# Kernel tuning notes

Hardware: AMD Instinct MI355X
Metric: run time of the kernel (lower is better)

Reference implementation:

```python
import jax, jax.numpy as jnp
import numpy as np

D = 1024
H = 4
HD = D // H
WIN = 128
NPMEM = 4
EPS = 1e-5


def _layernorm(x, g, b):
    mu = jnp.mean(x, axis=-1, keepdims=True)
    var = jnp.var(x, axis=-1, keepdims=True)
    return (x - mu) * jax.lax.rsqrt(var + EPS) * g + b


def _rotate_half(t):
    h = t.shape[-1] // 2
    return jnp.concatenate([-t[..., h:], t[..., :h]], axis=-1)


def setup_inputs() -> dict:
    key = jax.random.key(0)
    ks = jax.random.split(key, 20)
    B, L = 2, 4096
    s = 0.02
    inp = {
        'x': jax.random.normal(ks[0], (B, L, D), jnp.float32),
        'cos': jax.random.uniform(ks[1], (L + 8, HD), jnp.float32),
        'sin': jax.random.uniform(ks[2], (L + 8, HD), jnp.float32),
        'global_out': jax.random.normal(ks[3], (B, L, D), jnp.float32),
        'local_out': jax.random.normal(ks[4], (B, L, D), jnp.float32),
        'wq': jax.random.normal(ks[5], (D, D), jnp.float32) * s,
        'wk': jax.random.normal(ks[6], (D, D), jnp.float32) * s,
        'wv': jax.random.normal(ks[7], (D, D), jnp.float32) * s,
        'wo_attn': jax.random.normal(ks[8], (D, D), jnp.float32) * s,
        'pmem': jax.random.normal(ks[9], (1, NPMEM, D), jnp.float32),
        'gate_w': jax.random.normal(ks[10], (3 * D, 3 * D), jnp.float32) * s,
        'gate_b': jnp.zeros((3 * D,), jnp.float32),
        'outproj_w': jax.random.normal(ks[11], (3 * D, D), jnp.float32) * s,
        'outproj_b': jnp.zeros((D,), jnp.float32),
        'ln_mem_g': jnp.ones((D,), jnp.float32),
        'ln_mem_b': jnp.zeros((D,), jnp.float32),
        'ln_mlp_g': jnp.ones((D,), jnp.float32),
        'ln_mlp_b': jnp.zeros((D,), jnp.float32),
        'fc1_w': jax.random.normal(ks[12], (D, 4 * D), jnp.float32) * s,
        'fc1_b': jnp.zeros((4 * D,), jnp.float32),
        'fc2_w': jax.random.normal(ks[13], (4 * D, D), jnp.float32) * s,
        'fc2_b': jnp.zeros((D,), jnp.float32),
    }
    return inp


def reference(x, cos, sin, global_out, local_out, wq, wk, wv, wo_attn, pmem,
              gate_w, gate_b, outproj_w, outproj_b, ln_mem_g, ln_mem_b,
              ln_mlp_g, ln_mlp_b, fc1_w, fc1_b, fc2_w, fc2_b):
    B, L, _ = x.shape
    residual = x

    # prepend persistent memory tokens
    xp = jnp.concatenate([jnp.broadcast_to(pmem, (B, NPMEM, D)), x], axis=1)
    Lt = L + NPMEM

    q = (xp @ wq).reshape(B, Lt, H, HD)
    k = (xp @ wk).reshape(B, Lt, H, HD)
    v = (xp @ wv).reshape(B, Lt, H, HD)

    # rotary embedding over the full pmem+seq length
    cc = cos[:Lt][None, :, None, :]
    ss = sin[:Lt][None, :, None, :]
    q = q * cc + _rotate_half(q) * ss
    k = k * cc + _rotate_half(k) * ss

    i = jnp.arange(Lt)[:, None]
    j = jnp.arange(Lt)[None, :]
    mask = (j <= i) & (j >= i - WIN)  # [Lt, Lt]

    scale = 1.0 / jnp.sqrt(jnp.asarray(HD, x.dtype))
    scores = jnp.einsum('blhd,bmhd->bhlm', q, k) * scale
    scores = jnp.where(mask[None, None], scores, jnp.finfo(scores.dtype).min)
    attn = jax.nn.softmax(scores, axis=-1)
    out = jnp.einsum('bhlm,bmhd->blhd', attn, v).reshape(B, Lt, D)
    core_out = (out @ wo_attn)[:, -L:, :]

    combined = jnp.concatenate([global_out, local_out, core_out], axis=-1)
    g = jax.nn.sigmoid(combined @ gate_w + gate_b)
    memory_output = (combined * g) @ outproj_w + outproj_b

    x1 = residual + _layernorm(memory_output, ln_mem_g, ln_mem_b)
    xn = _layernorm(x1, ln_mlp_g, ln_mlp_b)
    mlp_out = jax.nn.silu(xn @ fc1_w + fc1_b) @ fc2_w + fc2_b
    return x1 + mlp_out
```

## Files before the change

### kernel.cpp

```cpp
#include <hip/hip_runtime.h>
#include <stdint.h>

#define D_    1024
#define H_    4
#define HD_   256
#define WIN_  128
#define NPM_  4
#define B_    2
#define L_    4096
#define LT_   4100
#define LTP_  4112
#define QKL_  3072

typedef __attribute__((ext_vector_type(8))) short short8;
typedef __attribute__((ext_vector_type(4))) float f32x4;

__device__ __forceinline__ short f2bf(float f) {
  union { float f; uint32_t u; } v; v.f = f;
  uint32_t r = v.u + 0x7FFFu + ((v.u >> 16) & 1u);
  return (short)(r >> 16);
}
__device__ __forceinline__ float bf2f(short h) {
  union { uint32_t u; float f; } v; v.u = ((uint32_t)(uint16_t)h) << 16;
  return v.f;
}

typedef __attribute__((address_space(1))) void GAS;
typedef __attribute__((address_space(3))) void LAS;
__device__ __forceinline__ void gl16(const void* g, void* l) {
  __builtin_amdgcn_global_load_lds((GAS*)g, (LAS*)l, 16, 0, 0);
}
__device__ __forceinline__ void waitvm0() { asm volatile("s_waitcnt vmcnt(0)" ::: "memory"); }

#define EP_BF16 0
#define EP_F32B 1
#define EP_GATE 2
#define EP_SILU 3
#define EP_RES  4
#define EP_CORE 5

template<int EP, int TM>
__global__ __launch_bounds__(256, 2)
void gemm_bt(const short* __restrict__ A, int lda,
             const short* __restrict__ Bt,
             void* __restrict__ Cp, int ldc,
             const float* __restrict__ bias,
             const void* __restrict__ aux, int ldaux,
             int M, int N, int K)
{
  constexpr int WM = TM / 2;
  constexpr int MT = WM / 16;
  constexpr int BUFSZ = (TM + 128) * 32;
  __shared__ __attribute__((aligned(16))) short lds[2 * BUFSZ];
  const int tid  = threadIdx.x;
  const int lane = tid & 63, wave = tid >> 6;
  const int lhi  = lane >> 4, llo = lane & 15;
  const int m0 = blockIdx.x * TM, n0 = blockIdx.y * 128;
  const int mw = (wave >> 1) * WM, nw = (wave & 1) * 64;

  const int srow = tid >> 2;
  const int sg   = (tid & 3) ^ ((tid >> 3) & 3);
  const short* pA0 = A + (size_t)min(m0 + srow, M - 1) * lda + sg * 8;
  const short* pA1 = (TM == 128) ? A + (size_t)min(m0 + srow + 64, M - 1) * lda + sg * 8 : pA0;
  const short* pB0 = Bt + (size_t)(n0 + srow) * K + sg * 8;
  const short* pB1 = Bt + (size_t)(n0 + srow + 64) * K + sg * 8;

  const int segoff = (lhi ^ ((llo >> 1) & 3)) * 8;

  auto stage = [&](int b, int i) {
    const int k = i << 5;
    short* base = &lds[b * BUFSZ];
    gl16(pA0 + k, &base[tid * 8]);
    if constexpr (TM == 128) gl16(pA1 + k, &base[2048 + tid * 8]);
    gl16(pB0 + k, &base[TM * 32 + tid * 8]);
    gl16(pB1 + k, &base[TM * 32 + 2048 + tid * 8]);
  };

  f32x4 acc[MT][4];
#pragma unroll
  for (int i = 0; i < MT; i++)
#pragma unroll
    for (int j = 0; j < 4; j++) acc[i][j] = f32x4{0.f, 0.f, 0.f, 0.f};

  const int NI = K >> 5;
  stage(0, 0);
  waitvm0();
  __syncthreads();

  for (int i = 0; i < NI; i++) {
    if (i + 1 < NI) stage((i + 1) & 1, i + 1);
    const short* bufp = &lds[(i & 1) * BUFSZ];
    short8 af[MT], bfr[4];
#pragma unroll
    for (int mt = 0; mt < MT; mt++)
      af[mt] = *(const short8*)&bufp[(mw + mt * 16 + llo) * 32 + segoff];
#pragma unroll
    for (int nt = 0; nt < 4; nt++)
      bfr[nt] = *(const short8*)&bufp[TM * 32 + (nw + nt * 16 + llo) * 32 + segoff];
#pragma unroll
    for (int mt = 0; mt < MT; mt++)
#pragma unroll
      for (int nt = 0; nt < 4; nt++)
        acc[mt][nt] = __builtin_amdgcn_mfma_f32_16x16x32_bf16(af[mt], bfr[nt], acc[mt][nt], 0, 0, 0);
    waitvm0();
    __syncthreads();
  }

  const int gcb = n0 + nw;
#pragma unroll
  for (int mt = 0; mt < MT; mt++) {
    const int gr0 = m0 + mw + mt * 16 + lhi * 4;
#pragma unroll
    for (int nt = 0; nt < 4; nt++) {
      const int gc = gcb + nt * 16 + llo;
      float bv = 0.f;
      if constexpr (EP != EP_BF16 && EP != EP_CORE) bv = bias[gc];
#pragma unroll
      for (int r = 0; r < 4; r++) {
        const int gr = gr0 + r;
        if (gr >= M) continue;
        const float v = acc[mt][nt][r];
        if constexpr (EP == EP_CORE) {
          const int b   = gr >= LT_ ? 1 : 0;
          const int tok = gr - b * LT_;
          if (tok >= NPM_) {
            const int cr = b * L_ + (tok - NPM_);
            ((short*)Cp)[(size_t)cr * ldc + gc] = f2bf(v);
          }
          continue;
        }
        const size_t idx = (size_t)gr * ldc + gc;
        if constexpr (EP == EP_BF16) {
          ((short*)Cp)[idx] = f2bf(v);
        } else if constexpr (EP == EP_F32B) {
          ((float*)Cp)[idx] = v + bv;
        } else if constexpr (EP == EP_GATE) {
          float g  = 1.f / (1.f + __expf(-(v + bv)));
          float cv = bf2f(((const short*)aux)[(size_t)gr * ldaux + gc]);
          ((short*)Cp)[idx] = f2bf(cv * g);
        } else if constexpr (EP == EP_SILU) {
          float xx = v + bv;
          ((short*)Cp)[idx] = f2bf(xx / (1.f + __expf(-xx)));
        } else {
          ((float*)Cp)[idx] = v + bv + ((const float*)aux)[(size_t)gr * ldaux + gc];
        }
      }
    }
  }
}

struct TAll {
  const float* src[8];
  short* dst[8];
  int C[8];
  int R[8];
  int nbx[8];
  int start[8];
};

__global__ __launch_bounds__(256)
void transpose_all(TAll t)
{
  __shared__ short tile[32][33];
  const int bid = blockIdx.x;
  int w = 0;
#pragma unroll
  for (int i = 1; i < 8; i++) w = (bid >= t.start[i]) ? i : w;
  const int rel = bid - t.start[w];
  const int nbx = t.nbx[w];
  const int bx = rel % nbx, by = rel / nbx;
  const float* src = t.src[w];
  short* dst = t.dst[w];
  const int ld_in = t.C[w], ld_out = t.R[w];
  const int r0 = by * 32, c0 = bx * 32;
  const int tx = threadIdx.x & 31, ty = threadIdx.x >> 5;
#pragma unroll
  for (int i = 0; i < 4; i++)
    tile[ty + i * 8][tx] = f2bf(src[(size_t)(r0 + ty + i * 8) * ld_in + c0 + tx]);
  __syncthreads();
#pragma unroll
  for (int i = 0; i < 4; i++)
    dst[(size_t)(c0 + ty + i * 8) * ld_out + r0 + tx] = tile[tx][ty + i * 8];
}

template<typename Tin>
__global__ __launch_bounds__(256)
void cast_transpose(const Tin* __restrict__ in, short* __restrict__ outp,
                    int R, int C, int ld_in, int ld_out,
                    int zdiv, size_t inA, size_t inB, size_t outA, size_t outB)
{
  __shared__ short tile[32][33];
  const int z = blockIdx.z;
  const Tin* src = in + (size_t)(z / zdiv) * inA + (size_t)(z % zdiv) * inB;
  short* dst = outp + (size_t)(z / zdiv) * outA + (size_t)(z % zdiv) * outB;
  const int r0 = blockIdx.y * 32, c0 = blockIdx.x * 32;
  const int tx = threadIdx.x & 31, ty = threadIdx.x >> 5;
#pragma unroll
  for (int i = 0; i < 4; i++) {
    int r = r0 + ty + i * 8, c = c0 + tx;
    short v = 0;
    if (r < R && c < C) {
      if constexpr (sizeof(Tin) == 4) v = f2bf((float)src[(size_t)r * ld_in + c]);
      else                            v = (short)src[(size_t)r * ld_in + c];
    }
    tile[ty + i * 8][tx] = v;
  }
  __syncthreads();
#pragma unroll
  for (int i = 0; i < 4; i++) {
    int c = c0 + ty + i * 8, r = r0 + tx;
    if (c < C && r < R) dst[(size_t)c * ld_out + r] = tile[tx][ty + i * 8];
  }
}

__global__ __launch_bounds__(256)
void build_xp_k(const float* __restrict__ x, const float* __restrict__ pmem,
                short* __restrict__ xp)
{
  int gid = blockIdx.x * 256 + threadIdx.x;
  int row = gid >> 8;
  int c4  = (gid & 255) * 4;
  int b   = row >= LT_ ? 1 : 0;
  int tok = row - b * LT_;
  const float* src = (tok < NPM_) ? (pmem + (size_t)tok * D_ + c4)
                                  : (x + ((size_t)b * L_ + tok - NPM_) * D_ + c4);
  float4 v = *(const float4*)src;
  short o[4] = {f2bf(v.x), f2bf(v.y), f2bf(v.z), f2bf(v.w)};
  *(short4*)&xp[(size_t)row * D_ + c4] = *(short4*)o;
}

__global__ __launch_bounds__(256)
void combined01_k(const float* __restrict__ go, const float* __restrict__ lo,
                  short* __restrict__ comb)
{
  int gid = blockIdx.x * 256 + threadIdx.x;
  int row = gid >> 9;
  int c4  = (gid & 511) * 4;
  const float* src = (c4 < D_) ? (go + (size_t)row * D_ + c4)
                               : (lo + (size_t)row * D_ + (c4 - D_));
  float4 v = *(const float4*)src;
  short o[4] = {f2bf(v.x), f2bf(v.y), f2bf(v.z), f2bf(v.w)};
  *(short4*)&comb[(size_t)row * 3072 + c4] = *(short4*)o;
}

__global__ __launch_bounds__(256)
void rope_kernel(short* __restrict__ qkv,
                 const float* __restrict__ cosp, const float* __restrict__ sinp)
{
  int gid = blockIdx.x * 256 + threadIdx.x;
  int d   = (gid & 31) * 4;
  int h   = (gid >> 5) & 3;
  int row = gid >> 7;
  int t   = row >= LT_ ? row - LT_ : row;
  size_t base = (size_t)row * QKL_ + h * HD_ + d;
  float4 cl = *(const float4*)&cosp[(size_t)t * HD_ + d];
  float4 ch = *(const float4*)&cosp[(size_t)t * HD_ + d + 128];
  float4 sl = *(const float4*)&sinp[(size_t)t * HD_ + d];
  float4 sh = *(const float4*)&sinp[(size_t)t * HD_ + d + 128];
  short4 ql4 = *(const short4*)&qkv[base],        qh4 = *(const short4*)&qkv[base + 128];
  short4 kl4 = *(const short4*)&qkv[base + 1024], kh4 = *(const short4*)&qkv[base + 1152];
  const float SC = 1.f / 16.f;
  short oql[4], oqh[4], okl[4], okh[4];
#pragma unroll
  for (int j = 0; j < 4; j++) {
    float c0 = ((float*)&cl)[j], c1 = ((float*)&ch)[j];
    float s0 = ((float*)&sl)[j], s1 = ((float*)&sh)[j];
    float ql = bf2f(((short*)&ql4)[j]), qh = bf2f(((short*)&qh4)[j]);
    float kl = bf2f(((short*)&kl4)[j]), kh = bf2f(((short*)&kh4)[j]);
    oql[j] = f2bf((ql * c0 - qh * s0) * SC);
    oqh[j] = f2bf((qh * c1 + ql * s1) * SC);
    okl[j] = f2bf(kl * c0 - kh * s0);
    okh[j] = f2bf(kh * c1 + kl * s1);
  }
  *(short4*)&qkv[base]        = *(short4*)oql;
  *(short4*)&qkv[base + 128]  = *(short4*)oqh;
  *(short4*)&qkv[base + 1024] = *(short4*)okl;
  *(short4*)&qkv[base + 1152] = *(short4*)okh;
}

__global__ __launch_bounds__(256, 1)
void attn_kernel(const short* __restrict__ qkv, const short* __restrict__ vT,
                 short* __restrict__ outp)
{
  __shared__ short lKV[256 * 72];
  __shared__ short lP[64 * 200];
  const int tid  = threadIdx.x;
  const int lane = tid & 63, wave = tid >> 6;
  const int lhi  = lane >> 4, llo = lane & 15;
  const int i0 = blockIdx.x * 64;
  const int h = blockIdx.y, b = blockIdx.z;
  const int kw0 = i0 - 128;
  const size_t vbase = (size_t)(b * H_ + h) * HD_ * LTP_;

  short8 qf[8];
  {
    int ic = min(i0 + wave * 16 + llo, LT_ - 1);
    const short* qrow = qkv + (size_t)(b * LT_ + ic) * QKL_ + h * HD_;
#pragma unroll
    for (int ks = 0; ks < 8; ks++)
      qf[ks] = *(const short8*)(qrow + ks * 32 + lhi * 8);
  }

  f32x4 S[12];
#pragma unroll
  for (int st = 0; st < 12; st++) S[st] = f32x4{0.f, 0.f, 0.f, 0.f};

  for (int kc = 0; kc < 3; kc++) {
    if (kc) __syncthreads();
    {
      int row = tid >> 2;
      int jc = min(max(kw0 + kc * 64 + row, 0), LT_ - 1);
      const short* krow = qkv + (size_t)(b * LT_ + jc) * QKL_ + 1024 + h * HD_;
#pragma unroll
      for (int it = 0; it < 8; it++) {
        int seg = (tid & 3) + it * 4;
        *(short8*)&lKV[row * 264 + seg * 8] = *(const short8*)(krow + seg * 8);
      }
    }
    __syncthreads();
#pragma unroll
    for (int ks = 0; ks < 8; ks++) {
#pragma unroll
      for (int nt = 0; nt < 4; nt++) {
        short8 bf = *(const short8*)&lKV[(nt * 16 + llo) * 264 + ks * 32 + lhi * 8];
        S[kc * 4 + nt] = __builtin_amdgcn_mfma_f32_16x16x32_bf16(qf[ks], bf, S[kc * 4 + nt], 0, 0, 0);
      }
    }
  }

  const int irow = i0 + wave * 16 + lhi * 4;
  float mx[4], sm[4];
#pragma unroll
  for (int r = 0; r < 4; r++) mx[r] = -3.0e38f;
#pragma unroll
  for (int st = 0; st < 12; st++) {
    int j = kw0 + st * 16 + llo;
#pragma unroll
    for (int r = 0; r < 4; r++) {
      int i = irow + r;
      bool ok = (j >= 0) & (j <= i) & (j >= i - WIN_);
      float s = ok ? S[st][r] : -1.0e30f;
      S[st][r] = s;
      mx[r] = fmaxf(mx[r], s);
    }
  }
#pragma unroll
  for (int r = 0; r < 4; r++)
#pragma unroll
    for (int o = 1; o < 16; o <<= 1) mx[r] = fmaxf(mx[r], __shfl_xor(mx[r], o));
#pragma unroll
  for (int r = 0; r < 4; r++) sm[r] = 0.f;
#pragma unroll
  for (int st = 0; st < 12; st++)
#pragma unroll
    for (int r = 0; r < 4; r++) {
      float e = __expf(S[st][r] - mx[r]);
      S[st][r] = e;
      sm[r] += e;
    }
#pragma unroll
  for (int r = 0; r < 4; r++) {
#pragma unroll
    for (int o = 1; o < 16; o <<= 1) sm[r] += __shfl_xor(sm[r], o);
    sm[r] = 1.f / sm[r];
  }

#pragma unroll
  for (int st = 0; st < 12; st++)
#pragma unroll
    for (int r = 0; r < 4; r++)
      lP[(wave * 16 + lhi * 4 + r) * 200 + st * 16 + llo] = f2bf(S[st][r] * sm[r]);

  f32x4 O[16];
#pragma unroll
  for (int nt = 0; nt < 16; nt++) O[nt] = f32x4{0.f, 0.f, 0.f, 0.f};

  for (int kc = 0; kc < 3; kc++) {
    __syncthreads();
#pragma unroll
    for (int it = 0; it < 8; it++) {
      int id = it * 256 + tid;
      int d = id >> 3, seg = id & 7;
      int kbase = min(max(kw0 + kc * 64 + seg * 8, 0), LTP_ - 8);
      *(short8*)&lKV[d * 72 + seg * 8] = *(const short8*)&vT[vbase + (size_t)d * LTP_ + kbase];
    }
    __syncthreads();
#pragma unroll
    for (int ks = 0; ks < 2; ks++) {
      short8 pf = *(const short8*)&lP[(wave * 16 + llo) * 200 + kc * 64 + ks * 32 + lhi * 8];
#pragma unroll
      for (int nt = 0; nt < 16; nt++) {
        short8 vf = *(const short8*)&lKV[(nt * 16 + llo) * 72 + ks * 32 + lhi * 8];
        O[nt] = __builtin_amdgcn_mfma_f32_16x16x32_bf16(pf, vf, O[nt], 0, 0, 0);
      }
    }
  }

  short* orow = outp + (size_t)(b * LT_) * D_ + h * HD_;
#pragma unroll
  for (int nt = 0; nt < 16; nt++)
#pragma unroll
    for (int r = 0; r < 4; r++) {
      int i = irow + r;
      if (i < LT_) orow[(size_t)i * D_ + nt * 16 + llo] = f2bf(O[nt][r]);
    }
}

__global__ __launch_bounds__(256, 4)
void ln2_kernel(const float* __restrict__ mo, const float* __restrict__ xres,
                const float* __restrict__ g1, const float* __restrict__ b1,
                const float* __restrict__ g2, const float* __restrict__ b2,
                float* __restrict__ x1, short* __restrict__ xn)
{
  const int row = blockIdx.x;
  const int tid = threadIdx.x;
  const int lane = tid & 63, wave = tid >> 6;
  __shared__ float red[8], red2[8];
  float4 v = ((const float4*)(mo + (size_t)row * D_))[tid];
  float s = v.x + v.y + v.z + v.w;
  float s2 = v.x * v.x + v.y * v.y + v.z * v.z + v.w * v.w;
#pragma unroll
  for (int o = 1; o < 64; o <<= 1) { s += __shfl_xor(s, o); s2 += __shfl_xor(s2, o); }
  if (lane == 0) { red[wave] = s; red[wave + 4] = s2; }
  __syncthreads();
  float S = red[0] + red[1] + red[2] + red[3];
  float S2 = red[4] + red[5] + red[6] + red[7];
  float mu = S * (1.f / D_);
  float rs = rsqrtf(S2 * (1.f / D_) - mu * mu + 1e-5f);
  float4 gg = ((const float4*)g1)[tid];
  float4 bb = ((const float4*)b1)[tid];
  float4 xv = ((const float4*)(xres + (size_t)row * D_))[tid];
  float4 o1;
  o1.x = xv.x + (v.x - mu) * rs * gg.x + bb.x;
  o1.y = xv.y + (v.y - mu) * rs * gg.y + bb.y;
  o1.z = xv.z + (v.z - mu) * rs * gg.z + bb.z;
  o1.w = xv.w + (v.w - mu) * rs * gg.w + bb.w;
  ((float4*)(x1 + (size_t)row * D_))[tid] = o1;
  s = o1.x + o1.y + o1.z + o1.w;
  s2 = o1.x * o1.x + o1.y * o1.y + o1.z * o1.z + o1.w * o1.w;
#pragma unroll
  for (int o = 1; o < 64; o <<= 1) { s += __shfl_xor(s, o); s2 += __shfl_xor(s2, o); }
  if (lane == 0) { red2[wave] = s; red2[wave + 4] = s2; }
  __syncthreads();
  S = red2[0] + red2[1] + red2[2] + red2[3];
  S2 = red2[4] + red2[5] + red2[6] + red2[7];
  float mu2 = S * (1.f / D_);
  float rs2 = rsqrtf(S2 * (1.f / D_) - mu2 * mu2 + 1e-5f);
  float4 g2v = ((const float4*)g2)[tid];
  float4 b2v = ((const float4*)b2)[tid];
  short o2[4];
  o2[0] = f2bf((o1.x - mu2) * rs2 * g2v.x + b2v.x);
  o2[1] = f2bf((o1.y - mu2) * rs2 * g2v.y + b2v.y);
  o2[2] = f2bf((o1.z - mu2) * rs2 * g2v.z + b2v.z);
  o2[3] = f2bf((o1.w - mu2) * rs2 * g2v.w + b2v.w);
  *(short4*)&xn[(size_t)row * D_ + tid * 4] = *(short4*)o2;
}

extern "C" void kernel_launch(void* const* d_in, const int* in_sizes, int n_in,
                              void* d_out, int out_size, void* d_ws, size_t ws_size,
                              hipStream_t stream)
{
  const float* x      = (const float*)d_in[0];
  const float* cosp   = (const float*)d_in[1];
  const float* sinp   = (const float*)d_in[2];
  const float* go     = (const float*)d_in[3];
  const float* lo     = (const float*)d_in[4];
  const float* wq     = (const float*)d_in[5];
  const float* wk     = (const float*)d_in[6];
  const float* wv     = (const float*)d_in[7];
  const float* wo     = (const float*)d_in[8];
  const float* pmem   = (const float*)d_in[9];
  const float* gate_w = (const float*)d_in[10];
  const float* gate_b = (const float*)d_in[11];
  const float* outp_w = (const float*)d_in[12];
  const float* outp_b = (const float*)d_in[13];
  const float* ln1g   = (const float*)d_in[14];
  const float* ln1b   = (const float*)d_in[15];
  const float* ln2g   = (const float*)d_in[16];
  const float* ln2b   = (const float*)d_in[17];
  const float* fc1w   = (const float*)d_in[18];
  const float* fc1b   = (const float*)d_in[19];
  const float* fc2w   = (const float*)d_in[20];
  const float* fc2b   = (const float*)d_in[21];
  float* out = (float*)d_out;
  char* p = (char*)d_ws;

  short* wqkvT = (short*)(p + 0);
  short* woT   = (short*)(p + 6291456);
  short* gateT = (short*)(p + 8388608);
  short* outpT = (short*)(p + 27262976);
  short* fc1T  = (short*)(p + 33554432);
  short* fc2T  = (short*)(p + 41943040);
  short* comb  = (short*)(p + 50331648);
  char*  pool  = p + 100663296;
  short* xp    = (short*)(pool);
  short* qkv   = (short*)(pool + 16793600);
  short* vT    = (short*)(pool + 67174400);
  short* a_o   = (short*)(pool + 84017152);
  short* gated = (short*)(pool);
  short* h1    = (short*)(pool);
  float* mo    = (float*)(pool + 67174400);
  float* x1    = (float*)(comb);
  short* xn    = (short*)((char*)comb + 33554432);

  TAll t;
  const float* srcs[8] = {wq, wk, wv, wo, gate_w, outp_w, fc1w, fc2w};
  short* dsts[8] = {wqkvT, wqkvT + 1048576, wqkvT + 2097152, woT, gateT, outpT, fc1T, fc2T};
  const int Rs[8] = {1024, 1024, 1024, 1024, 3072, 3072, 1024, 4096};
  const int Cs[8] = {1024, 1024, 1024, 1024, 3072, 1024, 4096, 1024};
  int cum = 0;
  for (int i = 0; i < 8; i++) {
    t.src[i] = srcs[i]; t.dst[i] = dsts[i];
    t.R[i] = Rs[i]; t.C[i] = Cs[i]; t.nbx[i] = Cs[i] / 32;
    t.start[i] = cum;
    cum += (Cs[i] / 32) * (Rs[i] / 32);
  }
  transpose_all<<<cum, 256, 0, stream>>>(t);

  build_xp_k<<<8200, 256, 0, stream>>>(x, pmem, xp);
  combined01_k<<<16384, 256, 0, stream>>>(go, lo, comb);

  const int Mq = B_ * LT_;
  gemm_bt<EP_BF16, 128><<<dim3(65, 24), 256, 0, stream>>>(xp, 1024, wqkvT, qkv, QKL_, nullptr, nullptr, 0, Mq, 3072, 1024);

  rope_kernel<<<4100, 256, 0, stream>>>(qkv, cosp, sinp);
  cast_transpose<short><<<dim3(8, 129, 8), 256, 0, stream>>>(
      qkv + 2048, vT, LT_, 256, QKL_, LTP_, 4,
      (size_t)LT_ * QKL_, 256, (size_t)4 * 256 * LTP_, (size_t)256 * LTP_);

  attn_kernel<<<dim3(65, H_, B_), 256, 0, stream>>>(qkv, vT, a_o);

  gemm_bt<EP_CORE, 64><<<dim3(129, 8), 256, 0, stream>>>(
      a_o, 1024, woT, comb + 2048, 3072, nullptr, nullptr, 0, Mq, 1024, 1024);

  gemm_bt<EP_GATE, 128><<<dim3(64, 24), 256, 0, stream>>>(comb, 3072, gateT, gated, 3072, gate_b, comb, 3072, 8192, 3072, 3072);

  gemm_bt<EP_F32B, 64><<<dim3(128, 8), 256, 0, stream>>>(gated, 3072, outpT, mo, 1024, outp_b, nullptr, 0, 8192, 1024, 3072);

  ln2_kernel<<<8192, 256, 0, stream>>>(mo, x, ln1g, ln1b, ln2g, ln2b, x1, xn);

  gemm_bt<EP_SILU, 128><<<dim3(64, 32), 256, 0, stream>>>(xn, 1024, fc1T, h1, 4096, fc1b, nullptr, 0, 8192, 4096, 1024);
  gemm_bt<EP_RES, 64><<<dim3(128, 8), 256, 0, stream>>>(h1, 4096, fc2T, out, 1024, fc2b, x1, 1024, 8192, 1024, 4096);
}
```

Measured before the change: 972.2 us.

## Compute V transposed directly via swapped GEMM and fuse prep kernels

The V projection is split out of the fused QKV GEMM and computed as Wv^T · xp^T, with a new epilogue that writes straight into the head-major transposed V buffer. This removes the separate cast_transpose pass and the V columns of the qkv buffer. The two input-conversion kernels are merged into one launch, and the launch-bounds occupancy hints for the GEMM and attention kernels are raised. The transposed-store epilogue writes with strided scatter, and the higher occupancy hints may cause register spills.

```diff
diff --git a/kernel.cpp b/kernel.cpp
--- a/kernel.cpp
+++ b/kernel.cpp
@@ -10,7 +10,7 @@
 #define L_    4096
 #define LT_   4100
 #define LTP_  4112
-#define QKL_  3072
+#define QKL_  2048
 
 typedef __attribute__((ext_vector_type(8))) short short8;
 typedef __attribute__((ext_vector_type(4))) float f32x4;
@@ -38,9 +38,10 @@
 #define EP_SILU 3
 #define EP_RES  4
 #define EP_CORE 5
+#define EP_VT   6
 
 template<int EP, int TM>
-__global__ __launch_bounds__(256, 2)
+__global__ __launch_bounds__(256, 4)
 void gemm_bt(const short* __restrict__ A, int lda,
              const short* __restrict__ Bt,
              void* __restrict__ Cp, int ldc,
@@ -114,12 +115,21 @@
     for (int nt = 0; nt < 4; nt++) {
       const int gc = gcb + nt * 16 + llo;
       float bv = 0.f;
-      if constexpr (EP != EP_BF16 && EP != EP_CORE) bv = bias[gc];
+      if constexpr (EP != EP_BF16 && EP != EP_CORE && EP != EP_VT) bv = bias[gc];
 #pragma unroll
       for (int r = 0; r < 4; r++) {
         const int gr = gr0 + r;
         if (gr >= M) continue;
         const float v = acc[mt][nt][r];
+        if constexpr (EP == EP_VT) {
+          if (gc < N) {
+            const int b   = gc >= LT_ ? 1 : 0;
+            const int tok = gc - b * LT_;
+            const int hh  = gr >> 8, dd = gr & 255;
+            ((short*)Cp)[(size_t)((b * H_ + hh) * HD_ + dd) * ldc + tok] = f2bf(v);
+          }
+          continue;
+        }
         if constexpr (EP == EP_CORE) {
           const int b   = gr >= LT_ ? 1 : 0;
           const int tok = gr - b * LT_;
@@ -183,64 +193,33 @@
     dst[(size_t)(c0 + ty + i * 8) * ld_out + r0 + tx] = tile[tx][ty + i * 8];
 }
 
-template<typename Tin>
 __global__ __launch_bounds__(256)
-void cast_transpose(const Tin* __restrict__ in, short* __restrict__ outp,
-                    int R, int C, int ld_in, int ld_out,
-                    int zdiv, size_t inA, size_t inB, size_t outA, size_t outB)
-{
-  __shared__ short tile[32][33];
-  const int z = blockIdx.z;
-  const Tin* src = in + (size_t)(z / zdiv) * inA + (size_t)(z % zdiv) * inB;
-  short* dst = outp + (size_t)(z / zdiv) * outA + (size_t)(z % zdiv) * outB;
-  const int r0 = blockIdx.y * 32, c0 = blockIdx.x * 32;
-  const int tx = threadIdx.x & 31, ty = threadIdx.x >> 5;
-#pragma unroll
-  for (int i = 0; i < 4; i++) {
-    int r = r0 + ty + i * 8, c = c0 + tx;
-    short v = 0;
-    if (r < R && c < C) {
-      if constexpr (sizeof(Tin) == 4) v = f2bf((float)src[(size_t)r * ld_in + c]);
-      else                            v = (short)src[(size_t)r * ld_in + c];
-    }
-    tile[ty + i * 8][tx] = v;
-  }
-  __syncthreads();
-#pragma unroll
-  for (int i = 0; i < 4; i++) {
-    int c = c0 + ty + i * 8, r = r0 + tx;
-    if (c < C && r < R) dst[(size_t)c * ld_out + r] = tile[tx][ty + i * 8];
-  }
-}
-
-__global__ __launch_bounds__(256)
-void build_xp_k(const float* __restrict__ x, const float* __restrict__ pmem,
-                short* __restrict__ xp)
-{
-  int gid = blockIdx.x * 256 + threadIdx.x;
-  int row = gid >> 8;
-  int c4  = (gid & 255) * 4;
-  int b   = row >= LT_ ? 1 : 0;
-  int tok = row - b * LT_;
-  const float* src = (tok < NPM_) ? (pmem + (size_t)tok * D_ + c4)
-                                  : (x + ((size_t)b * L_ + tok - NPM_) * D_ + c4);
-  float4 v = *(const float4*)src;
-  short o[4] = {f2bf(v.x), f2bf(v.y), f2bf(v.z), f2bf(v.w)};
-  *(short4*)&xp[(size_t)row * D_ + c4] = *(short4*)o;
-}
-
-__global__ __launch_bounds__(256)
-void combined01_k(const float* __restrict__ go, const float* __restrict__ lo,
-                  short* __restrict__ comb)
-{
-  int gid = blockIdx.x * 256 + threadIdx.x;
-  int row = gid >> 9;
-  int c4  = (gid & 511) * 4;
-  const float* src = (c4 < D_) ? (go + (size_t)row * D_ + c4)
-                               : (lo + (size_t)row * D_ + (c4 - D_));
-  float4 v = *(const float4*)src;
-  short o[4] = {f2bf(v.x), f2bf(v.y), f2bf(v.z), f2bf(v.w)};
-  *(short4*)&comb[(size_t)row * 3072 + c4] = *(short4*)o;
+void prep_k(const float* __restrict__ x, const float* __restrict__ pmem,
+            const float* __restrict__ go, const float* __restrict__ lo,
+            short* __restrict__ xp, short* __restrict__ comb)
+{
+  const int bid = blockIdx.x;
+  if (bid < 8200) {
+    int gid = bid * 256 + threadIdx.x;
+    int row = gid >> 8;
+    int c4  = (gid & 255) * 4;
+    int b   = row >= LT_ ? 1 : 0;
+    int tok = row - b * LT_;
+    const float* src = (tok < NPM_) ? (pmem + (size_t)tok * D_ + c4)
+                                    : (x + ((size_t)b * L_ + tok - NPM_) * D_ + c4);
+    float4 v = *(const float4*)src;
+    short o[4] = {f2bf(v.x), f2bf(v.y), f2bf(v.z), f2bf(v.w)};
+    *(short4*)&xp[(size_t)row * D_ + c4] = *(short4*)o;
+  } else {
+    int gid = (bid - 8200) * 256 + threadIdx.x;
+    int row = gid >> 9;
+    int c4  = (gid & 511) * 4;
+    const float* src = (c4 < D_) ? (go + (size_t)row * D_ + c4)
+                                 : (lo + (size_t)row * D_ + (c4 - D_));
+    float4 v = *(const float4*)src;
+    short o[4] = {f2bf(v.x), f2bf(v.y), f2bf(v.z), f2bf(v.w)};
+    *(short4*)&comb[(size_t)row * 3072 + c4] = *(short4*)o;
+  }
 }
 
 __global__ __launch_bounds__(256)
@@ -278,7 +257,7 @@
   *(short4*)&qkv[base + 1152] = *(short4*)okh;
 }
 
-__global__ __launch_bounds__(256, 1)
+__global__ __launch_bounds__(256, 2)
 void attn_kernel(const short* __restrict__ qkv, const short* __restrict__ vT,
                  short* __restrict__ outp)
 {
@@ -517,16 +496,13 @@
   }
   transpose_all<<<cum, 256, 0, stream>>>(t);
 
-  build_xp_k<<<8200, 256, 0, stream>>>(x, pmem, xp);
-  combined01_k<<<16384, 256, 0, stream>>>(go, lo, comb);
+  prep_k<<<24584, 256, 0, stream>>>(x, pmem, go, lo, xp, comb);
 
   const int Mq = B_ * LT_;
-  gemm_bt<EP_BF16, 128><<<dim3(65, 24), 256, 0, stream>>>(xp, 1024, wqkvT, qkv, QKL_, nullptr, nullptr, 0, Mq, 3072, 1024);
+  gemm_bt<EP_BF16, 128><<<dim3(65, 16), 256, 0, stream>>>(xp, 1024, wqkvT, qkv, QKL_, nullptr, nullptr, 0, Mq, 2048, 1024);
+  gemm_bt<EP_VT, 64><<<dim3(16, 65), 256, 0, stream>>>(wqkvT + 2097152, 1024, xp, vT, LTP_, nullptr, nullptr, 0, 1024, 8200, 1024);
 
   rope_kernel<<<4100, 256, 0, stream>>>(qkv, cosp, sinp);
-  cast_transpose<short><<<dim3(8, 129, 8), 256, 0, stream>>>(
-      qkv + 2048, vT, LT_, 256, QKL_, LTP_, 4,
-      (size_t)LT_ * QKL_, 256, (size_t)4 * 256 * LTP_, (size_t)256 * LTP_);
 
   attn_kernel<<<dim3(65, H_, B_), 256, 0, stream>>>(qkv, vT, a_o);
 
```

New measurement: 969.1 us. About the same (-0.3%).
